# Kernel optimization log

Hardware: AMD Instinct MI355X
Metric: run time of the kernel (lower is better)

Reference implementation:

```python
import jax, jax.numpy as jnp
import numpy as np
import itertools

K = 3            # kernel size
KSS = K * K      # kernel_space_size = 9
STRIDE = 1
PAD = 1
ORDERS = (1, 2)


def _unfold(x, k, stride, pad):
    """torch.nn.Unfold equivalent: [B,C,H,W] -> [B, C*k*k, L], feature order (c, kh, kw)."""
    B, C, H, W = x.shape
    xp = jnp.pad(x, ((0, 0), (0, 0), (pad, pad), (pad, pad)))
    oh = (H + 2 * pad - k) // stride + 1
    ow = (W + 2 * pad - k) // stride + 1
    rows = (jnp.arange(oh) * stride)[:, None] + jnp.arange(k)[None, :]  # [oh,k]
    cols = (jnp.arange(ow) * stride)[:, None] + jnp.arange(k)[None, :]  # [ow,k]
    # broadcast indices -> patches [B,C,oh,ow,k,k]
    p = xp[:, :, rows[:, None, :, None], cols[None, :, None, :]]
    p = p.transpose(0, 1, 4, 5, 2, 3).reshape(B, C * k * k, oh * ow)
    return p, oh, ow


def _superdiag_keep(kss, order):
    """Complement of VolterraKernel2d mask: True at sorted-combination positions."""
    keep = np.zeros((kss,) * order, dtype=bool)
    for idx in itertools.combinations_with_replacement(range(kss), order):
        keep[idx] = True
    return keep.reshape(-1)


def _volterra_features(xp4, order):
    """xp4: [B,C,L,kss] -> masked+scaled order-`order` features [B,C,L,kss**order]."""
    if order == 1:
        return xp4  # masking/scaling disabled for order 1 in the original
    f = xp4
    for _ in range(order - 1):
        f = jnp.einsum('bclp,bclq->bclpq', f, xp4)
        f = f.reshape(*f.shape[:3], -1)
    keep = _superdiag_keep(KSS, order)                 # static numpy bool
    scale = 1.0 / np.sqrt(keep.sum())                   # 1/sqrt(#kept) == original scaling_factor
    return f * jnp.asarray(keep, f.dtype) * jnp.asarray(scale, f.dtype)


def setup_inputs() -> dict:
    key = jax.random.key(0)
    k1, k2, k3 = jax.random.split(key, 3)
    B, C, H, W = 4, 64, 64, 64
    out_ch = 64
    x = jax.random.normal(k1, (B, C, H, W), dtype=jnp.float32)
    W1 = jax.random.normal(k2, (C * KSS, out_ch), dtype=jnp.float32) * 0.05
    W2 = jax.random.normal(k3, (C * KSS ** 2, out_ch), dtype=jnp.float32) * 0.02
    bias_w = jnp.zeros((out_ch, 1, 1), dtype=jnp.float32)
    return {"x": x, "W1": W1, "W2": W2, "bias_w": bias_w}


def reference(x, W1, W2, bias_w):
    B, C, H, W = x.shape
    unf, oh, ow = _unfold(x, K, STRIDE, PAD)           # [B, C*kss, L]
    L = oh * ow
    xp4 = unf.reshape(B, C, KSS, L).transpose(0, 1, 3, 2)  # [B,C,L,kss]
    out = 0.0
    for order, Wt in zip(ORDERS, (W1, W2)):
        f = _volterra_features(xp4, order)             # [B,C,L,kss**order]
        feat = f.transpose(0, 2, 1, 3).reshape(B, L, -1)   # [B,L,C*kss**order]
        out = out + feat @ Wt                          # [B,L,out_ch]
    out_ch = W1.shape[1]
    # faithful to the original: raw view of [B,L,out_ch] memory into [B,out_ch,oh,ow]
    out = out.reshape(B, out_ch, oh, ow) + bias_w
    return out
```

## Files before the change

kernel.cpp:

```cpp
#include <hip/hip_runtime.h>
#include <hip/hip_bf16.h>


typedef __bf16 bf16x8 __attribute__((ext_vector_type(8)));
typedef float f32x16 __attribute__((ext_vector_type(16)));

#define SCALE_Q 0.14907119849998599f

__device__ __constant__ int g_pairP[45] = {
  0,0,0,0,0,0,0,0,0, 1,1,1,1,1,1,1,1, 2,2,2,2,2,2,2,
  3,3,3,3,3,3, 4,4,4,4,4, 5,5,5,5, 6,6,6, 7,7, 8};
__device__ __constant__ int g_pairQ[45] = {
  0,1,2,3,4,5,6,7,8, 1,2,3,4,5,6,7,8, 2,3,4,5,6,7,8,
  3,4,5,6,7,8, 4,5,6,7,8, 5,6,7,8, 6,7,8, 7,8, 8};

union AFrag { unsigned int u[4]; bf16x8 v; };
union BFrag { uint4 q; bf16x8 v; };

__device__ inline unsigned int pack_bf16x2(float a, float b){
  union { __hip_bfloat16 h; unsigned short s; } ca, cb;
  ca.h = __float2bfloat16(a);
  cb.h = __float2bfloat16(b);
  return (unsigned int)ca.s | ((unsigned int)cb.s << 16);
}

__device__ inline void half_swap(unsigned int U, unsigned int V,
                                 unsigned int& o0, unsigned int& o1, int lane){
#if __has_builtin(__builtin_amdgcn_permlane32_swap)
  auto rr = __builtin_amdgcn_permlane32_swap(U, V, false, false);
  o0 = rr[0]; o1 = rr[1];
#else
  unsigned int Ux = (unsigned int)__shfl_xor((int)U, 32);
  unsigned int Vx = (unsigned int)__shfl_xor((int)V, 32);
  const bool hi = (lane >= 32);
  o0 = hi ? Vx : U;
  o1 = hi ? V : Ux;
#endif
}

__global__ __launch_bounds__(256) void volt_pack(const float* __restrict__ W1,
                                                 const float* __restrict__ W2,
                                                 __hip_bfloat16* __restrict__ Bpack){
  int g = blockIdx.x * 256 + threadIdx.x;
  int c     = g >> 9;
  int inner = g & 511;
  int lane  = inner & 63;
  int ks    = inner >> 7;
  int nb    = (inner >> 6) & 1;
  int n     = nb * 32 + (lane & 31);
  int kh    = lane >> 5;
  #pragma unroll
  for (int j = 0; j < 8; ++j){
    int f = ks * 16 + kh * 8 + j;
    float wv = 0.0f;
    if (f < 9)       wv = W1[(c * 9 + f) * 64 + n];
    else if (f < 54){
      int t = f - 9;
      wv = SCALE_Q * W2[(c * 81 + g_pairP[t] * 9 + g_pairQ[t]) * 64 + n];
    }
    Bpack[(size_t)g * 8 + j] = __float2bfloat16(wv);
  }
}

__global__ __launch_bounds__(512, 2) void volt_main(const float* __restrict__ x,
                                                    const uint4* __restrict__ Bpack,
                                                    const float* __restrict__ bias_w,
                                                    float* __restrict__ out){
  __shared__ float red[8 * 4096];
  const int tid  = threadIdx.x;
  const int lane = tid & 63;
  const int kv   = tid >> 6;
  const int b    = blockIdx.x >> 6;
  const int h0   = blockIdx.x & 63;

  const int hm = (h0 > 0)  ? (h0 - 1) : 0;
  const int hp = (h0 < 63) ? (h0 + 1) : 63;
  const float* xw = x + ((size_t)(b * 64 + kv * 8)) * 4096;
  const uint4* bsrc = Bpack + (size_t)(kv * 8) * 512 + lane;

  constexpr int kP[45] = {
    0,0,0,0,0,0,0,0,0, 1,1,1,1,1,1,1,1, 2,2,2,2,2,2,2,
    3,3,3,3,3,3, 4,4,4,4,4, 5,5,5,5, 6,6,6, 7,7, 8};
  constexpr int kQ[45] = {
    0,1,2,3,4,5,6,7,8, 1,2,3,4,5,6,7,8, 2,3,4,5,6,7,8,
    3,4,5,6,7,8, 4,5,6,7,8, 5,6,7,8, 6,7,8, 7,8, 8};

  f32x16 acc00{}, acc01{}, acc10{}, acc11{};

  BFrag curB[8];
  float cx[3];
  #pragma unroll
  for (int j = 0; j < 8; ++j) curB[j].q = bsrc[j * 64];
  cx[0] = xw[hm * 64 + lane];
  cx[1] = xw[h0 * 64 + lane];
  cx[2] = xw[hp * 64 + lane];

  #pragma unroll
  for (int i = 0; i < 8; ++i){
    BFrag nxtB[8];
    float nx2[3];
    if (i < 7){
      const uint4* s = bsrc + (size_t)(i + 1) * 512;
      #pragma unroll
      for (int j = 0; j < 8; ++j) nxtB[j].q = s[j * 64];
      const float* xc = xw + (size_t)(i + 1) * 4096;
      nx2[0] = xc[hm * 64 + lane];
      nx2[1] = xc[h0 * 64 + lane];
      nx2[2] = xc[hp * 64 + lane];
    }

    float xp[9];
    #pragma unroll
    for (int dh = 0; dh < 3; ++dh){
      float mid = cx[dh];
      if (dh == 0 && h0 == 0)  mid = 0.f;
      if (dh == 2 && h0 == 63) mid = 0.f;
      float lf = __shfl(mid, lane - 1);
      float rt = __shfl(mid, lane + 1);
      xp[dh * 3 + 0] = (lane == 0)  ? 0.f : lf;
      xp[dh * 3 + 1] = mid;
      xp[dh * 3 + 2] = (lane == 63) ? 0.f : rt;
    }
    float pr[45];
    #pragma unroll
    for (int t = 0; t < 45; ++t) pr[t] = xp[kP[t]] * xp[kQ[t]];

    unsigned int d[32];
    #pragma unroll
    for (int s = 0; s < 32; ++s){
      const int f0 = 2 * s, f1 = 2 * s + 1;
      float a  = (f0 < 9) ? xp[f0] : ((f0 < 54) ? pr[f0 - 9] : 0.0f);
      float b2 = (f1 < 9) ? xp[f1] : ((f1 < 54) ? pr[f1 - 9] : 0.0f);
      d[s] = pack_bf16x2(a, b2);
    }

    AFrag a0[4], a1[4];
    #pragma unroll
    for (int ks = 0; ks < 4; ++ks){
      #pragma unroll
      for (int j = 0; j < 4; ++j){
        half_swap(d[ks * 8 + j], d[ks * 8 + 4 + j], a0[ks].u[j], a1[ks].u[j], lane);
      }
    }

    #pragma unroll
    for (int ks = 0; ks < 4; ++ks){
      acc00 = __builtin_amdgcn_mfma_f32_32x32x16_bf16(a0[ks].v, curB[ks*2+0].v, acc00, 0, 0, 0);
      acc01 = __builtin_amdgcn_mfma_f32_32x32x16_bf16(a0[ks].v, curB[ks*2+1].v, acc01, 0, 0, 0);
      acc10 = __builtin_amdgcn_mfma_f32_32x32x16_bf16(a1[ks].v, curB[ks*2+0].v, acc10, 0, 0, 0);
      acc11 = __builtin_amdgcn_mfma_f32_32x32x16_bf16(a1[ks].v, curB[ks*2+1].v, acc11, 0, 0, 0);
    }

    if (i < 7){
      #pragma unroll
      for (int j = 0; j < 8; ++j) curB[j] = nxtB[j];
      cx[0] = nx2[0]; cx[1] = nx2[1]; cx[2] = nx2[2];
    }
  }

  {
    const int colbase = lane & 31;
    const int rowadd  = 4 * (lane >> 5);
    #pragma unroll
    for (int r = 0; r < 16; ++r){
      int rl = (r & 3) + 8 * (r >> 2) + rowadd;
      red[kv * 4096 + (rl)      * 64 + colbase     ] = acc00[r];
      red[kv * 4096 + (rl)      * 64 + colbase + 32] = acc01[r];
      red[kv * 4096 + (rl + 32) * 64 + colbase     ] = acc10[r];
      red[kv * 4096 + (rl + 32) * 64 + colbase + 32] = acc11[r];
    }
  }
  __syncthreads();
  const float bias = bias_w[h0];
  float* outp = out + (size_t)b * 262144 + (size_t)h0 * 4096;
  #pragma unroll
  for (int j = 0; j < 8; ++j){
    int oidx = j * 512 + tid;
    float v = bias;
    #pragma unroll
    for (int kvv = 0; kvv < 8; ++kvv) v += red[kvv * 4096 + oidx];
    outp[oidx] = v;
  }
}

extern "C" void kernel_launch(void* const* d_in, const int* in_sizes, int n_in,
                              void* d_out, int out_size, void* d_ws, size_t ws_size,
                              hipStream_t stream){
  const float* x      = (const float*)d_in[0];
  const float* W1     = (const float*)d_in[1];
  const float* W2     = (const float*)d_in[2];
  const float* bias_w = (const float*)d_in[3];
  float* out = (float*)d_out;
  __hip_bfloat16* Bpack = (__hip_bfloat16*)d_ws;

  volt_pack<<<128, 256, 0, stream>>>(W1, W2, Bpack);
  volt_main<<<256, 512, 0, stream>>>(x, (const uint4*)d_ws, bias_w, out);
}
```

Measured before the change: 22.66 us.

## Split each output row across two blocks and build A fragments per lane-half

Measured after the change: 31.03 us. +36.9%, slower.

```diff
diff --git a/kernel.cpp b/kernel.cpp
--- a/kernel.cpp
+++ b/kernel.cpp
@@ -14,6 +14,13 @@
   0,1,2,3,4,5,6,7,8, 1,2,3,4,5,6,7,8, 2,3,4,5,6,7,8,
   3,4,5,6,7,8, 4,5,6,7,8, 5,6,7,8, 6,7,8, 7,8, 8};
 
+constexpr int cP[45] = {
+  0,0,0,0,0,0,0,0,0, 1,1,1,1,1,1,1,1, 2,2,2,2,2,2,2,
+  3,3,3,3,3,3, 4,4,4,4,4, 5,5,5,5, 6,6,6, 7,7, 8};
+constexpr int cQ[45] = {
+  0,1,2,3,4,5,6,7,8, 1,2,3,4,5,6,7,8, 2,3,4,5,6,7,8,
+  3,4,5,6,7,8, 4,5,6,7,8, 5,6,7,8, 6,7,8, 7,8, 8};
+
 union AFrag { unsigned int u[4]; bf16x8 v; };
 union BFrag { uint4 q; bf16x8 v; };
 
@@ -24,18 +31,34 @@
   return (unsigned int)ca.s | ((unsigned int)cb.s << 16);
 }
 
-__device__ inline void half_swap(unsigned int U, unsigned int V,
-                                 unsigned int& o0, unsigned int& o1, int lane){
-#if __has_builtin(__builtin_amdgcn_permlane32_swap)
-  auto rr = __builtin_amdgcn_permlane32_swap(U, V, false, false);
-  o0 = rr[0]; o1 = rr[1];
-#else
-  unsigned int Ux = (unsigned int)__shfl_xor((int)U, 32);
-  unsigned int Vx = (unsigned int)__shfl_xor((int)V, 32);
-  const bool hi = (lane >= 32);
-  o0 = hi ? Vx : U;
-  o1 = hi ? V : Ux;
-#endif
+template<int F>
+__device__ inline float slotval(const float (&xp)[9]){
+  if constexpr (F < 9)       return xp[F];
+  else if constexpr (F < 54) return xp[cP[F - 9]] * xp[cQ[F - 9]];
+  else                       return 0.0f;
+}
+
+template<int KH>
+__device__ inline void build_afrag(const float (&xp)[9], AFrag (&a)[4]){
+  #pragma unroll
+  for (int ks = 0; ks < 4; ++ks){
+    #pragma unroll
+    for (int j = 0; j < 4; ++j){
+      constexpr int base = 0;  (void)base;
+      const int f0c = ks * 16 + KH * 8 + 2 * j;
+      float v0, v1;
+      switch (f0c) {
+        default: v0 = 0.f; v1 = 0.f; break;
+  #define CASE(F) case F: v0 = slotval<F>(xp); v1 = slotval<F+1>(xp); break;
+        CASE(0) CASE(2) CASE(4) CASE(6) CASE(8) CASE(10) CASE(12) CASE(14)
+        CASE(16) CASE(18) CASE(20) CASE(22) CASE(24) CASE(26) CASE(28) CASE(30)
+        CASE(32) CASE(34) CASE(36) CASE(38) CASE(40) CASE(42) CASE(44) CASE(46)
+        CASE(48) CASE(50) CASE(52) CASE(54) CASE(56) CASE(58) CASE(60) CASE(62)
+  #undef CASE
+      }
+      a[ks].u[j] = pack_bf16x2(v0, v1);
+    }
+  }
 }
 
 __global__ __launch_bounds__(256) void volt_pack(const float* __restrict__ W1,
@@ -62,123 +85,96 @@
   }
 }
 
-__global__ __launch_bounds__(512, 2) void volt_main(const float* __restrict__ x,
+__global__ __launch_bounds__(512, 4) void volt_main(const float* __restrict__ x,
                                                     const uint4* __restrict__ Bpack,
                                                     const float* __restrict__ bias_w,
                                                     float* __restrict__ out){
-  __shared__ float red[8 * 4096];
-  const int tid  = threadIdx.x;
-  const int lane = tid & 63;
-  const int kv   = tid >> 6;
-  const int b    = blockIdx.x >> 6;
-  const int h0   = blockIdx.x & 63;
+  __shared__ float red[8 * 2048];
+  const int tid   = threadIdx.x;
+  const int lane  = tid & 63;
+  const int kv    = tid >> 6;
+  const int bid   = blockIdx.x;
+  const int b     = bid >> 7;
+  const int h0    = (bid >> 1) & 63;
+  const int whalf = bid & 1;
+  const int wstart = whalf << 5;
 
-  const int hm = (h0 > 0)  ? (h0 - 1) : 0;
-  const int hp = (h0 < 63) ? (h0 + 1) : 63;
-  const float* xw = x + ((size_t)(b * 64 + kv * 8)) * 4096;
+  const int p  = lane & 31;
+  const int kh = lane >> 5;
+
+  const int hm = (h0 > 0)  ? h0 - 1 : 0;
+  const int hp = (h0 < 63) ? h0 + 1 : 63;
+
+  const float* xw  = x + ((size_t)(b * 64 + kv * 8)) * 4096;
   const uint4* bsrc = Bpack + (size_t)(kv * 8) * 512 + lane;
 
-  constexpr int kP[45] = {
-    0,0,0,0,0,0,0,0,0, 1,1,1,1,1,1,1,1, 2,2,2,2,2,2,2,
-    3,3,3,3,3,3, 4,4,4,4,4, 5,5,5,5, 6,6,6, 7,7, 8};
-  constexpr int kQ[45] = {
-    0,1,2,3,4,5,6,7,8, 1,2,3,4,5,6,7,8, 2,3,4,5,6,7,8,
-    3,4,5,6,7,8, 4,5,6,7,8, 5,6,7,8, 6,7,8, 7,8, 8};
+  const int col  = wstart - 1 + lane;
+  const bool cok = (lane < 34) && ((unsigned)col < 64u);
 
-  f32x16 acc00{}, acc01{}, acc10{}, acc11{};
+  auto loadX = [&](int i, float (&v)[3]){
+    const float* xc = xw + (size_t)i * 4096;
+    v[0] = cok ? xc[hm * 64 + col] : 0.f;
+    v[1] = cok ? xc[h0 * 64 + col] : 0.f;
+    v[2] = cok ? xc[hp * 64 + col] : 0.f;
+    if (h0 == 0)  v[0] = 0.f;
+    if (h0 == 63) v[2] = 0.f;
+  };
 
-  BFrag curB[8];
+  f32x16 acc0{}, acc1{};
   float cx[3];
-  #pragma unroll
-  for (int j = 0; j < 8; ++j) curB[j].q = bsrc[j * 64];
-  cx[0] = xw[hm * 64 + lane];
-  cx[1] = xw[h0 * 64 + lane];
-  cx[2] = xw[hp * 64 + lane];
+  loadX(0, cx);
 
   #pragma unroll
   for (int i = 0; i < 8; ++i){
-    BFrag nxtB[8];
+    BFrag Bf[8];
+    const uint4* s = bsrc + (size_t)i * 512;
+    #pragma unroll
+    for (int j = 0; j < 8; ++j) Bf[j].q = s[j * 64];
+
     float nx2[3];
-    if (i < 7){
-      const uint4* s = bsrc + (size_t)(i + 1) * 512;
-      #pragma unroll
-      for (int j = 0; j < 8; ++j) nxtB[j].q = s[j * 64];
-      const float* xc = xw + (size_t)(i + 1) * 4096;
-      nx2[0] = xc[hm * 64 + lane];
-      nx2[1] = xc[h0 * 64 + lane];
-      nx2[2] = xc[hp * 64 + lane];
-    }
+    if (i < 7) loadX(i + 1, nx2);
 
     float xp[9];
     #pragma unroll
     for (int dh = 0; dh < 3; ++dh){
-      float mid = cx[dh];
-      if (dh == 0 && h0 == 0)  mid = 0.f;
-      if (dh == 2 && h0 == 63) mid = 0.f;
-      float lf = __shfl(mid, lane - 1);
-      float rt = __shfl(mid, lane + 1);
-      xp[dh * 3 + 0] = (lane == 0)  ? 0.f : lf;
-      xp[dh * 3 + 1] = mid;
-      xp[dh * 3 + 2] = (lane == 63) ? 0.f : rt;
-    }
-    float pr[45];
-    #pragma unroll
-    for (int t = 0; t < 45; ++t) pr[t] = xp[kP[t]] * xp[kQ[t]];
-
-    unsigned int d[32];
-    #pragma unroll
-    for (int s = 0; s < 32; ++s){
-      const int f0 = 2 * s, f1 = 2 * s + 1;
-      float a  = (f0 < 9) ? xp[f0] : ((f0 < 54) ? pr[f0 - 9] : 0.0f);
-      float b2 = (f1 < 9) ? xp[f1] : ((f1 < 54) ? pr[f1 - 9] : 0.0f);
-      d[s] = pack_bf16x2(a, b2);
+      float hv = cx[dh];
+      xp[dh * 3 + 0] = __shfl(hv, p);
+      xp[dh * 3 + 1] = __shfl(hv, p + 1);
+      xp[dh * 3 + 2] = __shfl(hv, p + 2);
     }
 
-    AFrag a0[4], a1[4];
+    AFrag a[4];
+    if (kh == 0) build_afrag<0>(xp, a);
+    else         build_afrag<1>(xp, a);
+
+    __builtin_amdgcn_s_setprio(1);
     #pragma unroll
     for (int ks = 0; ks < 4; ++ks){
-      #pragma unroll
-      for (int j = 0; j < 4; ++j){
-        half_swap(d[ks * 8 + j], d[ks * 8 + 4 + j], a0[ks].u[j], a1[ks].u[j], lane);
-      }
+      acc0 = __builtin_amdgcn_mfma_f32_32x32x16_bf16(a[ks].v, Bf[ks*2+0].v, acc0, 0, 0, 0);
+      acc1 = __builtin_amdgcn_mfma_f32_32x32x16_bf16(a[ks].v, Bf[ks*2+1].v, acc1, 0, 0, 0);
     }
+    __builtin_amdgcn_s_setprio(0);
 
-    #pragma unroll
-    for (int ks = 0; ks < 4; ++ks){
-      acc00 = __builtin_amdgcn_mfma_f32_32x32x16_bf16(a0[ks].v, curB[ks*2+0].v, acc00, 0, 0, 0);
-      acc01 = __builtin_amdgcn_mfma_f32_32x32x16_bf16(a0[ks].v, curB[ks*2+1].v, acc01, 0, 0, 0);
-      acc10 = __builtin_amdgcn_mfma_f32_32x32x16_bf16(a1[ks].v, curB[ks*2+0].v, acc10, 0, 0, 0);
-      acc11 = __builtin_amdgcn_mfma_f32_32x32x16_bf16(a1[ks].v, curB[ks*2+1].v, acc11, 0, 0, 0);
-    }
-
-    if (i < 7){
-      #pragma unroll
-      for (int j = 0; j < 8; ++j) curB[j] = nxtB[j];
-      cx[0] = nx2[0]; cx[1] = nx2[1]; cx[2] = nx2[2];
-    }
+    if (i < 7){ cx[0] = nx2[0]; cx[1] = nx2[1]; cx[2] = nx2[2]; }
   }
 
   {
-    const int colbase = lane & 31;
-    const int rowadd  = 4 * (lane >> 5);
     #pragma unroll
     for (int r = 0; r < 16; ++r){
-      int rl = (r & 3) + 8 * (r >> 2) + rowadd;
-      red[kv * 4096 + (rl)      * 64 + colbase     ] = acc00[r];
-      red[kv * 4096 + (rl)      * 64 + colbase + 32] = acc01[r];
-      red[kv * 4096 + (rl + 32) * 64 + colbase     ] = acc10[r];
-      red[kv * 4096 + (rl + 32) * 64 + colbase + 32] = acc11[r];
+      int rl = (r & 3) + 8 * (r >> 2) + 4 * kh;
+      red[kv * 2048 + rl * 64 + p     ] = acc0[r];
+      red[kv * 2048 + rl * 64 + p + 32] = acc1[r];
     }
   }
   __syncthreads();
   const float bias = bias_w[h0];
-  float* outp = out + (size_t)b * 262144 + (size_t)h0 * 4096;
+  float* outp = out + (size_t)b * 262144 + (size_t)h0 * 4096 + (size_t)wstart * 64;
   #pragma unroll
-  for (int j = 0; j < 8; ++j){
+  for (int j = 0; j < 4; ++j){
     int oidx = j * 512 + tid;
     float v = bias;
     #pragma unroll
-    for (int kvv = 0; kvv < 8; ++kvv) v += red[kvv * 4096 + oidx];
+    for (int kvv = 0; kvv < 8; ++kvv) v += red[kvv * 2048 + oidx];
     outp[oidx] = v;
   }
 }
@@ -194,5 +190,5 @@
   __hip_bfloat16* Bpack = (__hip_bfloat16*)d_ws;
 
   volt_pack<<<128, 256, 0, stream>>>(W1, W2, Bpack);
-  volt_main<<<256, 512, 0, stream>>>(x, (const uint4*)d_ws, bias_w, out);
+  volt_main<<<512, 512, 0, stream>>>(x, (const uint4*)d_ws, bias_w, out);
 }
```
